# Kernel optimization log

Hardware: AMD Instinct MI355X
Metric: run time of the kernel (lower is better)

Reference implementation:

```python
import jax, jax.numpy as jnp
import numpy as np

B, C, V = 65536, 2, 3          # batch of coords, coord_dim, value_dim
D, K, S = 64, 1024, 4          # latent_dim, num_codes, num_latent_vectors (VQ stages)
H, L, F = 1024, 5, 25          # hidden_size, num_layers, num_freqs
IN = C * (2 * F + 1)           # 102: positional-encoded decoder input
COMMIT = 0.25


def setup_inputs() -> dict:
    key = jax.random.key(0)
    ks = jax.random.split(key, 12)
    coords = jax.random.uniform(ks[0], (B, C), jnp.float32, -1.0, 1.0)
    latents = jax.random.normal(ks[1], (1, S, D), jnp.float32)
    cb = jax.random.normal(ks[2], (S, K, D), jnp.float32)
    codebooks = cb / jnp.linalg.norm(cb, axis=-1, keepdims=True)  # unit-norm init as in module
    mod_W = jax.random.normal(ks[3], (L, D, H), jnp.float32) / np.sqrt(D)
    mod_b = jax.random.normal(ks[4], (L, H), jnp.float32) * 0.01
    dec_W0 = jax.random.normal(ks[5], (IN, H), jnp.float32) / np.sqrt(IN)
    dec_b0 = jax.random.normal(ks[6], (H,), jnp.float32) * 0.01
    dec_Wh = jax.random.normal(ks[7], (L - 1, H, H), jnp.float32) / np.sqrt(H)
    dec_bh = jax.random.normal(ks[8], (L - 1, H), jnp.float32) * 0.01
    dec_Wout = jax.random.normal(ks[9], (H, V), jnp.float32) / np.sqrt(H)
    dec_bout = jax.random.normal(ks[10], (V,), jnp.float32) * 0.01
    return dict(coords=coords, latent_idx=0, latents=latents, codebooks=codebooks,
                mod_W=mod_W, mod_b=mod_b, dec_W0=dec_W0, dec_b0=dec_b0,
                dec_Wh=dec_Wh, dec_bh=dec_bh, dec_Wout=dec_Wout, dec_bout=dec_bout)


def _vq(z, emb):
    # z: (1, D), emb: (K, D) -> squared-distance argmin + straight-through
    d = jnp.sum(z * z, axis=1, keepdims=True) - 2.0 * (z @ emb.T) + jnp.sum(emb * emb, axis=1)
    idx = jnp.argmin(d, axis=1)               # (1,)
    z_q = emb[idx]                            # (1, D)
    z_q_st = z_q + jax.lax.stop_gradient(z - z_q)   # fwd value == z, grad flows to embedding
    loss = COMMIT * jnp.mean((jax.lax.stop_gradient(z_q) - z) ** 2)
    return z_q_st, idx, loss


def reference(coords, latent_idx, latents, codebooks, mod_W, mod_b,
              dec_W0, dec_b0, dec_Wh, dec_bh, dec_Wout, dec_bout):
    img = latents[latent_idx]                 # (S, D)
    z_q_sum = jnp.zeros((1, D), coords.dtype)
    residual_target = jnp.zeros((1, D), coords.dtype)
    total_vq_loss = 0.0
    idxs = []
    for s in range(S):                        # residual VQ over fixed small #stages
        z_stage = img[s:s + 1]
        if s == 0:
            residual_target = z_stage
            z_cur = z_stage
        else:
            residual_target = residual_target + z_stage
            z_cur = residual_target - jax.lax.stop_gradient(z_q_sum)
        z_q_st, idx, l = _vq(z_cur, codebooks[s])
        z_q_sum = z_q_sum + z_q_st
        total_vq_loss = total_vq_loss + l
        idxs.append(idx)
    # modulation betas from the (same-for-all-rows) quantized latent; broadcast over B
    betas = jnp.einsum('od,ldh->loh', z_q_sum, mod_W) + mod_b[:, None, :]   # (L, 1, H)
    # positional encoding: [x, sin(pi*f0*x), cos(pi*f0*x), sin(pi*f1*x), ...]
    freqs = 2.0 ** jnp.arange(F, dtype=coords.dtype)
    ang = coords[:, None, :] * (freqs[None, :, None] * jnp.pi)              # (B, F, C)
    pe = jnp.concatenate(
        [coords, jnp.stack([jnp.sin(ang), jnp.cos(ang)], axis=2).reshape(coords.shape[0], -1)],
        axis=-1)                                                            # (B, IN)
    h = jax.nn.relu(pe @ dec_W0 + dec_b0 + betas[0])
    for i in range(L - 1):
        h = jax.nn.relu(h @ dec_Wh[i] + dec_bh[i] + betas[i + 1])
    values = h @ dec_Wout + dec_bout                                        # (B, V)
    return values, jnp.stack(idxs), total_vq_loss
```

## Files before the change

### kernel.cpp

```cpp
#include <hip/hip_runtime.h>
#include <hip/hip_bf16.h>
#include <stdint.h>

#define NB   65536
#define NC   2
#define NV   3
#define ND   64
#define NK   1024
#define NS   4
#define NH   1024
#define NL   5
#define NF   25
#define NIN  102
#define K0P  128

typedef float f32x4  __attribute__((ext_vector_type(4)));
typedef float f32x16 __attribute__((ext_vector_type(16)));
typedef int   i32x4  __attribute__((ext_vector_type(4)));
typedef int   i32x8  __attribute__((ext_vector_type(8)));
typedef unsigned char u8;

__device__ __forceinline__ void load_lds16(const void* g, void* l) {
    __builtin_amdgcn_global_load_lds(
        (const __attribute__((address_space(1))) void*)g,
        (__attribute__((address_space(3))) void*)l,
        16, 0, 0);
}

__device__ __forceinline__ u8 to_fp8(float x) {
    return (u8)(__builtin_amdgcn_cvt_pk_fp8_f32(x, 0.0f, 0, false) & 0xff);
}

__device__ __forceinline__ f32x16 mfma32(i32x8 wf, i32x8 af, f32x16 c) {
    return __builtin_amdgcn_mfma_scale_f32_32x32x64_f8f6f4(
        wf, af, c, 0, 0,
        0, 0x79797979,
        0, 0x7f7f7f7f);
}


__global__ __launch_bounds__(1024) void vq_kernel(
    const float* __restrict__ latents, const int* __restrict__ latent_idx,
    const float* __restrict__ codebooks, float* __restrict__ zq_out,
    float* __restrict__ out) {
    __shared__ float zcur[ND], resid[ND], zqsum[ND], ssq[ND];
    __shared__ float sDw[16];
    __shared__ int   sKw[16];
    __shared__ int   sBest;
    int t = threadIdx.x, lane = t & 63, wv = t >> 6;
    const float* img = latents + (size_t)latent_idx[0] * (NS * ND);
    if (t < ND) { resid[t] = 0.f; zqsum[t] = 0.f; }
    __syncthreads();
    float lossAcc = 0.f;
    for (int s = 0; s < NS; s++) {
        if (t < ND) {
            float iv = img[s * ND + t];
            float r  = resid[t] + iv;
            resid[t] = r;
            zcur[t]  = (s == 0) ? iv : (r - zqsum[t]);
        }
        __syncthreads();
        float zz = 0.f;
#pragma unroll
        for (int d = 0; d < ND; d++) { float z = zcur[d]; zz += z * z; }
        const float4* e4 = (const float4*)(codebooks + ((size_t)s * NK + t) * ND);
        float dot = 0.f, ee = 0.f;
#pragma unroll
        for (int i = 0; i < 16; i++) {
            float4 v = e4[i];
            dot += zcur[4 * i + 0] * v.x; dot += zcur[4 * i + 1] * v.y;
            dot += zcur[4 * i + 2] * v.z; dot += zcur[4 * i + 3] * v.w;
            ee  += v.x * v.x; ee += v.y * v.y; ee += v.z * v.z; ee += v.w * v.w;
        }
        float dmin = zz - 2.0f * dot + ee;
        int   kmin = t;
#pragma unroll
        for (int m = 1; m < 64; m <<= 1) {
            float d2 = __shfl_xor(dmin, m);
            int   k2 = __shfl_xor(kmin, m);
            if (d2 < dmin || (d2 == dmin && k2 < kmin)) { dmin = d2; kmin = k2; }
        }
        if (lane == 0) { sDw[wv] = dmin; sKw[wv] = kmin; }
        __syncthreads();
        if (t == 0) {
            float bd = sDw[0]; int bk = sKw[0];
            for (int w = 1; w < 16; w++) {
                float d2 = sDw[w]; int k2 = sKw[w];
                if (d2 < bd || (d2 == bd && k2 < bk)) { bd = d2; bk = k2; }
            }
            sBest = bk;
            out[NB * NV + s] = (float)bk;
        }
        __syncthreads();
        int best = sBest;
        const float* eb = codebooks + ((size_t)s * NK + best) * ND;
        if (t < ND) {
            float zq = eb[t];
            float d  = zq - zcur[t];
            ssq[t]   = d * d;
            zqsum[t] = zqsum[t] + (zq + (zcur[t] - zq));
        }
        __syncthreads();
        if (t < 64) {
            float sum = ssq[t];
#pragma unroll
            for (int m = 1; m < 64; m <<= 1) sum += __shfl_xor(sum, m);
            if (t == 0) lossAcc += 0.25f * (sum / (float)ND);
        }
    }
    if (t < ND) zq_out[t] = zqsum[t];
    if (t == 0) out[NB * NV + NS] = lossAcc;
}

__global__ __launch_bounds__(256) void betas_init_kernel(
    const float* __restrict__ zq, const float* __restrict__ mod_W,
    const float* __restrict__ mod_b, const float* __restrict__ b0,
    const float* __restrict__ bh, float* __restrict__ bb,
    const float* __restrict__ bout, float* __restrict__ out) {
    int g = blockIdx.x * 256 + threadIdx.x;
    if (g < 5120) {
        int l = g >> 10, n = g & 1023;
        float acc = mod_b[g];
        for (int d = 0; d < ND; d++) acc += zq[d] * mod_W[(size_t)(l * ND + d) * NH + n];
        acc += (l == 0) ? b0[n] : bh[(size_t)(l - 1) * NH + n];
        bb[g] = acc;
    } else {
        int o = g - 5120;
        if (o < NB * NV) out[o] = bout[o % NV];
    }
}

__global__ __launch_bounds__(256) void prep_kernel(
    const float* __restrict__ dec_W0, const float* __restrict__ dec_Wh,
    u8* __restrict__ W0T, u8* __restrict__ WhT) {
    int z = blockIdx.z;
    const float* src; u8* dst; int Ks, Kp;
    if (z < 4) {
        src = dec_Wh + (size_t)z * NH * NH; dst = WhT + (size_t)z * NH * NH;
        Ks = NH; Kp = NH;
    } else {
        if (blockIdx.x >= 4) return;
        src = dec_W0; dst = W0T; Ks = NIN; Kp = K0P;
    }
    __shared__ float tile[32][33];
    int k0 = blockIdx.x * 32, n0 = blockIdx.y * 32;
    int tx = threadIdx.x, ty = threadIdx.y;
    for (int i = 0; i < 4; i++) {
        int k = k0 + ty + i * 8;
        int n = n0 + tx;
        tile[ty + i * 8][tx] = (k < Ks) ? src[(size_t)k * NH + n] : 0.0f;
    }
    __syncthreads();
    for (int i = 0; i < 4; i++) {
        int n = n0 + ty + i * 8;
        int k = k0 + tx;
        int bn = n >> 7, j32 = (n >> 5) & 3, r32 = n & 31;
        int ks = k >> 6, kh = (k >> 5) & 1, h = (k >> 4) & 1, b16 = k & 15;
        size_t flat = (size_t)bn * ((size_t)Kp * 128)
                    + ((size_t)(((ks * 4 + j32) * 2 + h) * 2 + kh) * 32 + r32) * 16 + b16;
        dst[flat] = to_fp8(tile[tx][ty + i * 8] * 64.0f);
    }
}

__device__ __forceinline__ float pe_val(const float* coords, int m, int k) {
    if (k < 2) return coords[m * 2 + k];
    if (k >= NIN) return 0.0f;
    int u = k - 2;
    int f = u >> 2, r = u & 3;
    float c = coords[m * 2 + (r & 1)];
    float a = c * __builtin_ldexpf(3.14159274101257324f, f);
    return (r < 2) ? sinf(a) : cosf(a);
}

__global__ __launch_bounds__(256) void pe_kernel(
    const float* __restrict__ coords, u8* __restrict__ pe) {
    int g = blockIdx.x * 256 + threadIdx.x;
    int m = g >> 5, k4 = (g & 31) * 4;
    float v0 = pe_val(coords, m, k4 + 0);
    float v1 = pe_val(coords, m, k4 + 1);
    float v2 = pe_val(coords, m, k4 + 2);
    float v3 = pe_val(coords, m, k4 + 3);
    int p = __builtin_amdgcn_cvt_pk_fp8_f32(v0, v1, 0, false);
    p     = __builtin_amdgcn_cvt_pk_fp8_f32(v2, v3, p, true);
    int m32 = m >> 5, r32 = m & 31;
    int ks = k4 >> 6, kh = (k4 >> 5) & 1, h = (k4 >> 4) & 1, b16 = k4 & 15;
    *(int*)(pe + (size_t)(m32 * 2 + ks) * 2048
            + ((h * 2 + kh) * 32 + r32) * 16 + b16) = p;
}

template <int MODE, int KT>
__global__ __launch_bounds__(256, 2) void gemm_kernel(
    const u8* __restrict__ A, const u8* __restrict__ W,
    const float* __restrict__ bb, u8* __restrict__ O,
    const float* __restrict__ Wout, float* __restrict__ out, int Mb) {
    __shared__ __align__(16) u8 smem[32768];
    int t   = threadIdx.x;
    int fid = blockIdx.x;
    int xcd = fid & 7;
    int j8  = fid >> 3;
    int bn  = j8 & 7;
    int bm  = xcd * (Mb >> 3) + (j8 >> 3);
    int lane = t & 63, wm = t >> 6;
    int r32  = lane & 31, hl = lane >> 5;
    constexpr int nIt = KT >> 7;
    constexpr int nKs = KT >> 6;

    const u8* wslab = W + (size_t)bn * ((size_t)KT * 128);
    const u8* abase = A + ((size_t)(bm * 8 + wm * 2) * nKs) * 2048 + lane * 16;

    f32x16 acc[2][4];
#pragma unroll
    for (int i = 0; i < 2; i++)
#pragma unroll
        for (int j = 0; j < 4; j++)
#pragma unroll
            for (int e = 0; e < 16; e++) acc[i][j][e] = 0.0f;

#define LOAD_AF(dst, KS)                                                       \
    {                                                                          \
        _Pragma("unroll")                                                      \
        for (int mt = 0; mt < 2; mt++) {                                       \
            const u8* p = abase + ((size_t)mt * nKs + (KS)) * 2048;            \
            i32x4 lo = *(const i32x4*)(p);                                     \
            i32x4 hi = *(const i32x4*)(p + 1024);                              \
            dst[mt] = __builtin_shufflevector(lo, hi, 0, 1, 2, 3, 4, 5, 6, 7); \
        }                                                                      \
    }
#define MFMA_HALF(base, KSL, AF)                                               \
    {                                                                          \
        _Pragma("unroll")                                                      \
        for (int j = 0; j < 4; j++) {                                          \
            const u8* c = (base) + (KSL) * 8192 + j * 2048 + lane * 16;        \
            i32x4 lo = *(const i32x4*)(c);                                     \
            i32x4 hi = *(const i32x4*)(c + 1024);                              \
            i32x8 wf = __builtin_shufflevector(lo, hi, 0, 1, 2, 3, 4, 5, 6, 7);\
            acc[0][j] = mfma32(wf, AF[0], acc[0][j]);                          \
            acc[1][j] = mfma32(wf, AF[1], acc[1][j]);                          \
        }                                                                      \
    }

    if constexpr (nIt == 1) {
#pragma unroll
        for (int p = 0; p < 4; p++) {
            int g = p * 256 + t;
            load_lds16((const void*)(wslab + g * 16), (void*)(smem + g * 16));
        }
        i32x8 af0[2], af1[2];
        LOAD_AF(af0, 0)
        LOAD_AF(af1, 1)
        __syncthreads();
        MFMA_HALF(smem, 0, af0)
        MFMA_HALF(smem, 1, af1)
        __syncthreads();
    } else {
#pragma unroll
        for (int p = 0; p < 4; p++) {
            int g = p * 256 + t;
            load_lds16((const void*)(wslab + g * 16), (void*)(smem + g * 16));
        }
        i32x8 afc0[2], afc1[2], afn0[2], afn1[2];
        LOAD_AF(afc0, 0)
        LOAD_AF(afc1, 1)
        __syncthreads();

#pragma unroll 1
        for (int it = 0; it < nIt; it++) {
            u8* bufc = smem + ((it & 1) ? 16384 : 0);
            u8* bufn = smem + ((it & 1) ? 0 : 16384);
            if (it + 1 < nIt) {
                const u8* ws = wslab + (size_t)(it + 1) * 16384;
#pragma unroll
                for (int p = 0; p < 4; p++) {
                    int g = p * 256 + t;
                    load_lds16((const void*)(ws + g * 16), (void*)(bufn + g * 16));
                }
                LOAD_AF(afn0, 2 * (it + 1))
                LOAD_AF(afn1, 2 * (it + 1) + 1)
                asm volatile("" ::: "memory");
            }
            MFMA_HALF(bufc, 0, afc0)
            MFMA_HALF(bufc, 1, afc1)
            __syncthreads();
#pragma unroll
            for (int mt = 0; mt < 2; mt++) { afc0[mt] = afn0[mt]; afc1[mt] = afn1[mt]; }
        }
    }
#undef LOAD_AF
#undef MFMA_HALF

    if constexpr (MODE == 0) {
        u8* eb = smem;
#pragma unroll
        for (int mt = 0; mt < 2; mt++) {
#pragma unroll
            for (int nt = 0; nt < 4; nt++) {
                int kh  = nt & 1;
                int seg = (wm * 2 + mt) * 2 + (nt >> 1);
#pragma unroll
                for (int g = 0; g < 4; g++) {
                    int nbase = nt * 32 + 8 * g + 4 * hl;
                    f32x4 b4 = *(const f32x4*)(bb + bn * 128 + nbase);
                    float v0 = fmaxf(acc[mt][nt][4 * g + 0] + b4[0], 0.0f);
                    float v1 = fmaxf(acc[mt][nt][4 * g + 1] + b4[1], 0.0f);
                    float v2 = fmaxf(acc[mt][nt][4 * g + 2] + b4[2], 0.0f);
                    float v3 = fmaxf(acc[mt][nt][4 * g + 3] + b4[3], 0.0f);
                    int p = __builtin_amdgcn_cvt_pk_fp8_f32(v0, v1, 0, false);
                    p     = __builtin_amdgcn_cvt_pk_fp8_f32(v2, v3, p, true);
                    int h   = g >> 1;
                    int idx = seg * 2048 + ((h * 2 + kh) * 32 + r32) * 16
                            + ((8 * g + 4 * hl) & 15);
                    *(int*)(eb + idx) = p;
                }
            }
        }
        __syncthreads();
#pragma unroll
        for (int rd = 0; rd < 8; rd++) {
            int g2  = rd * 256 + t;
            int seg = g2 >> 7, off = (g2 & 127) * 16;
            int m32l = seg >> 1, ksl = seg & 1;
            i32x4 v = *(const i32x4*)(eb + seg * 2048 + off);
            *(i32x4*)(O + ((size_t)((bm * 8 + m32l) * (NH >> 6) + bn * 2 + ksl)) * 2048
                      + off) = v;
        }
    } else {
#pragma unroll
        for (int mt = 0; mt < 2; mt++) {
            float p0 = 0.f, p1 = 0.f, p2 = 0.f;
#pragma unroll
            for (int nt = 0; nt < 4; nt++) {
#pragma unroll
                for (int g = 0; g < 4; g++) {
                    int nbase = bn * 128 + nt * 32 + 8 * g + 4 * hl;
                    f32x4 b4 = *(const f32x4*)(bb + nbase);
#pragma unroll
                    for (int rr = 0; rr < 4; rr++) {
                        float val = fmaxf(acc[mt][nt][4 * g + rr] + b4[rr], 0.0f);
                        const float* wo = Wout + (size_t)(nbase + rr) * NV;
                        p0 += val * wo[0]; p1 += val * wo[1]; p2 += val * wo[2];
                    }
                }
            }
            p0 += __shfl_xor(p0, 32);
            p1 += __shfl_xor(p1, 32);
            p2 += __shfl_xor(p2, 32);
            if (hl == 0) {
                int m = bm * 256 + wm * 64 + mt * 32 + r32;
                atomicAdd(&out[(size_t)m * NV + 0], p0);
                atomicAdd(&out[(size_t)m * NV + 1], p1);
                atomicAdd(&out[(size_t)m * NV + 2], p2);
            }
        }
    }
}

extern "C" void kernel_launch(void* const* d_in, const int* in_sizes, int n_in,
                              void* d_out, int out_size, void* d_ws, size_t ws_size,
                              hipStream_t stream) {
    const float* coords     = (const float*)d_in[0];
    const int*   latent_idx = (const int*)d_in[1];
    const float* latents    = (const float*)d_in[2];
    const float* codebooks  = (const float*)d_in[3];
    const float* mod_W      = (const float*)d_in[4];
    const float* mod_b      = (const float*)d_in[5];
    const float* dec_W0     = (const float*)d_in[6];
    const float* dec_b0     = (const float*)d_in[7];
    const float* dec_Wh     = (const float*)d_in[8];
    const float* dec_bh     = (const float*)d_in[9];
    const float* dec_Wout   = (const float*)d_in[10];
    const float* dec_bout   = (const float*)d_in[11];
    float* out = (float*)d_out;

    char* wsb = (char*)d_ws;
    float* zq  = (float*)(wsb + 0);
    float* bb  = (float*)(wsb + 256);
    u8*    W0T = (u8*)(wsb + 20736);
    u8*    WhT = (u8*)(wsb + 151808);
    const size_t fixed_end = 4346368;

    int Bc = 65536;
    while (Bc > 2048 && fixed_end + 2 * (size_t)Bc * NH > ws_size)
        Bc >>= 1;
    int Mb = Bc / 256;

    u8* hA = (u8*)(wsb + fixed_end);
    u8* hB = hA + (size_t)Bc * NH;
    u8* pe = hB;

    vq_kernel<<<1, 1024, 0, stream>>>(latents, latent_idx, codebooks, zq, out);
    betas_init_kernel<<<(5120 + NB * NV) / 256, 256, 0, stream>>>(
        zq, mod_W, mod_b, dec_b0, dec_bh, bb, dec_bout, out);
    prep_kernel<<<dim3(32, 32, 5), dim3(32, 8), 0, stream>>>(
        dec_W0, dec_Wh, W0T, WhT);

    for (int c0 = 0; c0 < NB; c0 += Bc) {
        pe_kernel<<<(Bc * 32) / 256, 256, 0, stream>>>(coords + (size_t)c0 * NC, pe);
        gemm_kernel<0, K0P><<<8 * Mb, 256, 0, stream>>>(
            pe, W0T, bb + 0 * NH, hA, nullptr, nullptr, Mb);
        gemm_kernel<0, NH><<<8 * Mb, 256, 0, stream>>>(
            hA, WhT + 0 * (size_t)NH * NH, bb + 1 * NH, hB, nullptr, nullptr, Mb);
        gemm_kernel<0, NH><<<8 * Mb, 256, 0, stream>>>(
            hB, WhT + 1 * (size_t)NH * NH, bb + 2 * NH, hA, nullptr, nullptr, Mb);
        gemm_kernel<0, NH><<<8 * Mb, 256, 0, stream>>>(
            hA, WhT + 2 * (size_t)NH * NH, bb + 3 * NH, hB, nullptr, nullptr, Mb);
        gemm_kernel<1, NH><<<8 * Mb, 256, 0, stream>>>(
            hB, WhT + 3 * (size_t)NH * NH, bb + 4 * NH, nullptr,
            dec_Wout, out + (size_t)c0 * NV, Mb);
    }
}
```

Before: 473.5 us.

## Load weight fragments directly from global memory instead of LDS double-buffering

Drops the LDS staging of weight tiles (global_load_lds with double buffering and barriers) and has each wave load its weight fragments straight from global memory into registers before the MFMAs. The loop is unrolled by two and all __syncthreads in the main loop are gone. This removes barrier and LDS traffic overhead, but every wave now fetches the same weight slab separately, which relies on L2/L1 hits and loses the explicit prefetch overlap.

```diff
diff --git a/kernel.cpp b/kernel.cpp
--- a/kernel.cpp
+++ b/kernel.cpp
@@ -19,13 +19,6 @@
 typedef int   i32x4  __attribute__((ext_vector_type(4)));
 typedef int   i32x8  __attribute__((ext_vector_type(8)));
 typedef unsigned char u8;
-
-__device__ __forceinline__ void load_lds16(const void* g, void* l) {
-    __builtin_amdgcn_global_load_lds(
-        (const __attribute__((address_space(1))) void*)g,
-        (__attribute__((address_space(3))) void*)l,
-        16, 0, 0);
-}
 
 __device__ __forceinline__ u8 to_fp8(float x) {
     return (u8)(__builtin_amdgcn_cvt_pk_fp8_f32(x, 0.0f, 0, false) & 0xff);
@@ -205,7 +198,7 @@
     constexpr int nIt = KT >> 7;
     constexpr int nKs = KT >> 6;
 
-    const u8* wslab = W + (size_t)bn * ((size_t)KT * 128);
+    const u8* wslab = W + (size_t)bn * ((size_t)KT * 128) + lane * 16;
     const u8* abase = A + ((size_t)(bm * 8 + wm * 2) * nKs) * 2048 + lane * 16;
 
     f32x16 acc[2][4];
@@ -216,77 +209,32 @@
 #pragma unroll
             for (int e = 0; e < 16; e++) acc[i][j][e] = 0.0f;
 
-#define LOAD_AF(dst, KS)                                                       \
+#define LOAD_PAIR_G(dst, base)                                                 \
     {                                                                          \
-        _Pragma("unroll")                                                      \
-        for (int mt = 0; mt < 2; mt++) {                                       \
-            const u8* p = abase + ((size_t)mt * nKs + (KS)) * 2048;            \
-            i32x4 lo = *(const i32x4*)(p);                                     \
-            i32x4 hi = *(const i32x4*)(p + 1024);                              \
-            dst[mt] = __builtin_shufflevector(lo, hi, 0, 1, 2, 3, 4, 5, 6, 7); \
-        }                                                                      \
-    }
-#define MFMA_HALF(base, KSL, AF)                                               \
-    {                                                                          \
-        _Pragma("unroll")                                                      \
-        for (int j = 0; j < 4; j++) {                                          \
-            const u8* c = (base) + (KSL) * 8192 + j * 2048 + lane * 16;        \
-            i32x4 lo = *(const i32x4*)(c);                                     \
-            i32x4 hi = *(const i32x4*)(c + 1024);                              \
-            i32x8 wf = __builtin_shufflevector(lo, hi, 0, 1, 2, 3, 4, 5, 6, 7);\
-            acc[0][j] = mfma32(wf, AF[0], acc[0][j]);                          \
-            acc[1][j] = mfma32(wf, AF[1], acc[1][j]);                          \
-        }                                                                      \
-    }
-
-    if constexpr (nIt == 1) {
-#pragma unroll
-        for (int p = 0; p < 4; p++) {
-            int g = p * 256 + t;
-            load_lds16((const void*)(wslab + g * 16), (void*)(smem + g * 16));
-        }
-        i32x8 af0[2], af1[2];
-        LOAD_AF(af0, 0)
-        LOAD_AF(af1, 1)
-        __syncthreads();
-        MFMA_HALF(smem, 0, af0)
-        MFMA_HALF(smem, 1, af1)
-        __syncthreads();
-    } else {
-#pragma unroll
-        for (int p = 0; p < 4; p++) {
-            int g = p * 256 + t;
-            load_lds16((const void*)(wslab + g * 16), (void*)(smem + g * 16));
-        }
-        i32x8 afc0[2], afc1[2], afn0[2], afn1[2];
-        LOAD_AF(afc0, 0)
-        LOAD_AF(afc1, 1)
-        __syncthreads();
-
-#pragma unroll 1
-        for (int it = 0; it < nIt; it++) {
-            u8* bufc = smem + ((it & 1) ? 16384 : 0);
-            u8* bufn = smem + ((it & 1) ? 0 : 16384);
-            if (it + 1 < nIt) {
-                const u8* ws = wslab + (size_t)(it + 1) * 16384;
-#pragma unroll
-                for (int p = 0; p < 4; p++) {
-                    int g = p * 256 + t;
-                    load_lds16((const void*)(ws + g * 16), (void*)(bufn + g * 16));
-                }
-                LOAD_AF(afn0, 2 * (it + 1))
-                LOAD_AF(afn1, 2 * (it + 1) + 1)
-                asm volatile("" ::: "memory");
-            }
-            MFMA_HALF(bufc, 0, afc0)
-            MFMA_HALF(bufc, 1, afc1)
-            __syncthreads();
-#pragma unroll
-            for (int mt = 0; mt < 2; mt++) { afc0[mt] = afn0[mt]; afc1[mt] = afn1[mt]; }
-        }
-    }
-#undef LOAD_AF
-#undef MFMA_HALF
+        i32x4 lo_ = *(const i32x4*)(base);                                     \
+        i32x4 hi_ = *(const i32x4*)((base) + 1024);                            \
+        dst = __builtin_shufflevector(lo_, hi_, 0, 1, 2, 3, 4, 5, 6, 7);       \
+    }
+
+#pragma unroll 2
+    for (int it = 0; it < nIt; it++) {
+#pragma unroll
+        for (int ksl = 0; ksl < 2; ksl++) {
+            int ks = 2 * it + ksl;
+            i32x8 af0, af1;
+            LOAD_PAIR_G(af0, abase + ((size_t)(0 * nKs + ks)) * 2048)
+            LOAD_PAIR_G(af1, abase + ((size_t)(1 * nKs + ks)) * 2048)
+            const u8* wk = wslab + (size_t)ks * 8192;
+#pragma unroll
+            for (int j = 0; j < 4; j++) {
+                i32x8 wf;
+                LOAD_PAIR_G(wf, wk + j * 2048)
+                acc[0][j] = mfma32(wf, af0, acc[0][j]);
+                acc[1][j] = mfma32(wf, af1, acc[1][j]);
+            }
+        }
+    }
+#undef LOAD_PAIR_G
 
     if constexpr (MODE == 0) {
         u8* eb = smem;
```

After: 515.8 us. 9.0% more time.
